# Kernel optimization log

Hardware: AMD Instinct MI355X
Metric: run time of the kernel (lower is better)

## Reference

```python
import jax, jax.numpy as jnp
import numpy as np

SPATIAL_SHAPES = [(128, 128), (64, 64), (32, 32), (16, 16)]
D_MODEL = 256
N_HEADS = 8
N_LEVELS = 4
N_POINTS = 4
HEAD_DIM = D_MODEL // N_HEADS
B = 2
LEN_Q = sum(h * w for h, w in SPATIAL_SHAPES)  # 21760
LEN_IN = LEN_Q


def setup_inputs() -> dict:
    key = jax.random.key(0)
    ks = jax.random.split(key, 11)
    s = 1.0 / np.sqrt(D_MODEL).astype(np.float32)
    query = jax.random.normal(ks[0], (B, LEN_Q, D_MODEL), jnp.float32)
    reference_points = jax.random.uniform(ks[1], (B, LEN_Q, N_LEVELS, 2), jnp.float32)
    input_flatten = jax.random.normal(ks[2], (B, LEN_IN, D_MODEL), jnp.float32)
    W_off = jax.random.normal(ks[3], (D_MODEL, N_HEADS * N_LEVELS * N_POINTS * 2), jnp.float32) * s
    b_off = jnp.zeros((N_HEADS * N_LEVELS * N_POINTS * 2,), jnp.float32)
    W_attn = jax.random.normal(ks[4], (D_MODEL, N_HEADS * N_LEVELS * N_POINTS), jnp.float32) * s
    b_attn = jnp.zeros((N_HEADS * N_LEVELS * N_POINTS,), jnp.float32)
    W_val = jax.random.normal(ks[5], (D_MODEL, D_MODEL), jnp.float32) * s
    b_val = jnp.zeros((D_MODEL,), jnp.float32)
    W_out = jax.random.normal(ks[6], (D_MODEL, D_MODEL), jnp.float32) * s
    b_out = jnp.zeros((D_MODEL,), jnp.float32)
    return {"query": query, "reference_points": reference_points, "input_flatten": input_flatten,
            "W_off": W_off, "b_off": b_off, "W_attn": W_attn, "b_attn": b_attn,
            "W_val": W_val, "b_val": b_val, "W_out": W_out, "b_out": b_out}


def _ms_deform_core(value, sampling_locations, attention_weights):
    # value: (B, H, Dh, N_total); sampling_locations: (B, Lq, H, L, P, 2) in [0,1]
    # attention_weights: (B, Lq, H, L*P)
    Bv, Hn, Dh, _ = value.shape
    Lq = sampling_locations.shape[1]
    P = sampling_locations.shape[4]
    BN = Bv * Hn
    grids = 2.0 * sampling_locations - 1.0
    splits = np.cumsum([h * w for h, w in SPATIAL_SHAPES])[:-1].tolist()
    value_list = jnp.split(value, splits, axis=3)
    sampled_levels = []
    for lid, (Hh, Ww) in enumerate(SPATIAL_SHAPES):
        # (BN, H*W, Dh)
        val_flat = jnp.transpose(value_list[lid].reshape(BN, Dh, Hh * Ww), (0, 2, 1))
        # (BN, Lq, P, 2)
        g = jnp.transpose(grids[:, :, :, lid, :, :], (0, 2, 1, 3, 4)).reshape(BN, Lq, P, 2)
        ix = ((g[..., 0] + 1.0) * Ww - 1.0) / 2.0
        iy = ((g[..., 1] + 1.0) * Hh - 1.0) / 2.0
        ix0 = jnp.floor(ix).astype(jnp.int32)
        iy0 = jnp.floor(iy).astype(jnp.int32)
        ix1 = ix0 + 1
        iy1 = iy0 + 1
        fx = (ix - ix0.astype(ix.dtype))[..., None]
        fy = (iy - iy0.astype(iy.dtype))[..., None]

        def valid(yy, xx):
            return ((xx >= 0) & (xx < Ww) & (yy >= 0) & (yy < Hh)).astype(val_flat.dtype)[..., None]

        def gather(yy, xx):
            idx = (jnp.clip(yy, 0, Hh - 1) * Ww + jnp.clip(xx, 0, Ww - 1)).reshape(BN, Lq * P)
            out = jnp.take_along_axis(val_flat, idx[:, :, None], axis=1)
            return out.reshape(BN, Lq, P, Dh)

        v00 = gather(iy0, ix0) * valid(iy0, ix0)
        v01 = gather(iy0, ix1) * valid(iy0, ix1)
        v10 = gather(iy1, ix0) * valid(iy1, ix0)
        v11 = gather(iy1, ix1) * valid(iy1, ix1)
        sampled = ((1 - fx) * (1 - fy) * v00 + fx * (1 - fy) * v01
                   + (1 - fx) * fy * v10 + fx * fy * v11)  # (BN, Lq, P, Dh)
        sampled_levels.append(jnp.transpose(sampled, (0, 3, 1, 2)))  # (BN, Dh, Lq, P)
    # (BN, Dh, Lq, L*P)
    sv = jnp.stack(sampled_levels, axis=-2).reshape(BN, Dh, Lq, N_LEVELS * P)
    attn = jnp.transpose(attention_weights, (0, 2, 1, 3)).reshape(BN, 1, Lq, N_LEVELS * P)
    out = jnp.sum(sv * attn, axis=-1)  # (BN, Dh, Lq)
    out = out.reshape(Bv, Hn * Dh, Lq)
    return jnp.transpose(out, (0, 2, 1))  # (B, Lq, d_model)


def reference(query, reference_points, input_flatten, W_off, b_off, W_attn, b_attn, W_val, b_val, W_out, b_out):
    Bq, Lq, _ = query.shape
    Len_in = input_flatten.shape[1]
    value = input_flatten @ W_val + b_val  # (B, Len_in, d_model)
    offsets = (query @ W_off + b_off).reshape(Bq, Lq, N_HEADS, N_LEVELS, N_POINTS, 2)
    attn = jax.nn.softmax((query @ W_attn + b_attn).reshape(Bq, Lq, N_HEADS, N_LEVELS * N_POINTS), axis=-1)
    # normalizer is (W, H) per level
    offset_normalizer = jnp.asarray([[w, h] for h, w in SPATIAL_SHAPES], dtype=query.dtype)
    sampling_locations = (reference_points[:, :, None, :, None, :]
                          + offsets / offset_normalizer[None, None, None, :, None, :])
    value = jnp.transpose(value, (0, 2, 1)).reshape(Bq, N_HEADS, HEAD_DIM, Len_in)
    out = _ms_deform_core(value, sampling_locations, attn)
    return out @ W_out + b_out
```

## Files before the change

kernel.cpp:

```cpp
#include <hip/hip_runtime.h>
#include <hip/hip_bf16.h>
#include <hip/hip_fp16.h>
#include <type_traits>

#define B_    2
#define LQ_   21760
#define LEN_  21760
#define DM    256
#define NH    8
#define NL    4
#define NP    4
#define HD    32

#define WS_VAL   0u
#define WS_SAMP  22282240u
#define WS_OA    44564480u
#define WS_WT    77987840u

typedef __attribute__((ext_vector_type(4))) float f32x4;
typedef __attribute__((ext_vector_type(8))) short bf16x8;
typedef __attribute__((ext_vector_type(4))) unsigned int u32x4;
typedef __attribute__((ext_vector_type(2))) unsigned int u32x2;

__device__ __forceinline__ unsigned short f2bf(float v) {
    __hip_bfloat16 h = __float2bfloat16(v);
    return *reinterpret_cast<unsigned short*>(&h);
}
__device__ __forceinline__ unsigned int pk2bf(float a, float b) {
    return (unsigned int)f2bf(a) | ((unsigned int)f2bf(b) << 16);
}
__device__ __forceinline__ unsigned int pk2h(float a, float b) {
    __half2 h = __floats2half2_rn(a, b);
    union { __half2 h; unsigned int u; } c; c.h = h; return c.u;
}
__device__ __forceinline__ __half2 u2h2(unsigned int u) {
    union { unsigned int u; __half2 h; } c; c.u = u; return c.h;
}

__global__ __launch_bounds__(256) void wt_cvt_all(const float* __restrict__ Wv,
                                                  const float* __restrict__ Wo,
                                                  const float* __restrict__ Wa,
                                                  const float* __restrict__ Wu,
                                                  unsigned short* __restrict__ wt) {
    const float* Ws[4] = {Wv, Wo, Wa, Wu};
    const int Ns[4] = {256, 256, 128, 256};
    const unsigned int dof[4] = {0u, 65536u, 131072u, 163840u};
    const int m = blockIdx.z;
    const int n0 = blockIdx.x * 16, k0 = blockIdx.y * 16;
    if (n0 >= Ns[m]) return;
    __shared__ float tile[16][17];
    const int tx = threadIdx.x & 15, ty = threadIdx.x >> 4;
    tile[ty][tx] = Ws[m][(size_t)(k0 + ty) * Ns[m] + n0 + tx];
    __syncthreads();
    wt[dof[m] + (size_t)(n0 + ty) * 256 + k0 + tx] = f2bf(tile[tx][ty]);
}

__global__ __launch_bounds__(256) void gemm_pre(const float* __restrict__ inpf,
                                                const float* __restrict__ query,
                                                const unsigned short* __restrict__ Wt_val,
                                                const unsigned short* __restrict__ Wt_oa,
                                                const float* __restrict__ b_val,
                                                const float* __restrict__ b_off,
                                                const float* __restrict__ b_attn,
                                                unsigned short* __restrict__ val_h,
                                                unsigned short* __restrict__ oa_h) {
    __shared__ unsigned short As[128 * 32];
    __shared__ unsigned short Bs[128 * 32];
    const int t = threadIdx.x;
    const int wv = t >> 6;
    const int ln = t & 63;
    const int job = (blockIdx.x >= 2);
    const int n0 = (job ? (blockIdx.x - 2) : blockIdx.x) * 128;
    const int m0 = blockIdx.y * 128;
    const float* A = job ? query : inpf;
    const unsigned short* Bt = job ? Wt_oa : Wt_val;
    const int K = 256;
    const int wm = (wv & 1) * 64;
    const int wn = (wv >> 1) * 64;
    const int lrow = ln & 15;
    const int kq = ln >> 4;

    f32x4 acc[4][4] = {};

    for (int k0 = 0; k0 < K; k0 += 32) {
#pragma unroll
        for (int c = 0; c < 4; ++c) {
            const int i = t + c * 256;
            const int row = i >> 3;
            const int kq4 = (i & 7) * 4;
            f32x4 v = *(const f32x4*)&A[(size_t)(m0 + row) * K + k0 + kq4];
            uint2 p = make_uint2(pk2bf(v.x, v.y), pk2bf(v.z, v.w));
            *(uint2*)((char*)As + row * 64 + kq4 * 2) = p;
        }
#pragma unroll
        for (int c = 0; c < 2; ++c) {
            const int o = c * 4096 + t * 16;
            const int row = o >> 6;
            const int ke = (o & 63) >> 1;
            const unsigned short* gb = Bt + (size_t)(n0 + row) * K + k0 + ke;
            __builtin_amdgcn_global_load_lds(
                (const __attribute__((address_space(1))) void*)gb,
                (__attribute__((address_space(3))) void*)((char*)Bs + o), 16, 0, 0);
        }
        __syncthreads();

        bf16x8 af[4], bfr[4];
#pragma unroll
        for (int i = 0; i < 4; ++i) {
            af[i]  = *(const bf16x8*)((char*)As + (wm + i * 16 + lrow) * 64 + kq * 16);
            bfr[i] = *(const bf16x8*)((char*)Bs + (wn + i * 16 + lrow) * 64 + kq * 16);
        }
#pragma unroll
        for (int i = 0; i < 4; ++i)
#pragma unroll
            for (int j = 0; j < 4; ++j)
                acc[i][j] = __builtin_amdgcn_mfma_f32_16x16x32_bf16(af[i], bfr[j], acc[i][j], 0, 0, 0);
        __syncthreads();
    }

    const int b = m0 / LQ_;
#pragma unroll
    for (int j = 0; j < 4; ++j) {
        const int n = n0 + wn + j * 16 + lrow;
        const float bb = job ? ((n < 256) ? b_off[n] : b_attn[n - 256]) : b_val[n];
#pragma unroll
        for (int i = 0; i < 4; ++i) {
            const int mrow = m0 + wm + i * 16 + kq * 4;
#pragma unroll
            for (int r = 0; r < 4; ++r) {
                const float v = acc[i][j][r] + bb;
                const unsigned short hv = (unsigned short)__half_as_ushort(__float2half(v));
                if (job) {
                    oa_h[(size_t)(mrow + r) * 384 + n] = hv;
                } else {
                    const int pix = (mrow + r) - b * LQ_;
                    const int h = n >> 5, c = n & 31;
                    val_h[((size_t)(b * NH + h) * LQ_ + pix) * HD + c] = hv;
                }
            }
        }
    }
}

__global__ __launch_bounds__(256) void gemm_out(const unsigned short* __restrict__ Ab,
                                                const unsigned short* __restrict__ Bt,
                                                const float* __restrict__ bias,
                                                float* __restrict__ C) {
    __shared__ unsigned short As[128 * 32];
    __shared__ unsigned short Bs[128 * 32];
    const int t = threadIdx.x;
    const int wv = t >> 6;
    const int ln = t & 63;
    const int n0 = blockIdx.x * 128;
    const int m0 = blockIdx.y * 128;
    const int N = 256, K = 256;
    const int wm = (wv & 1) * 64;
    const int wn = (wv >> 1) * 64;
    const int lrow = ln & 15;
    const int kq = ln >> 4;

    f32x4 acc[4][4] = {};

    for (int k0 = 0; k0 < K; k0 += 32) {
#pragma unroll
        for (int c = 0; c < 2; ++c) {
            const int o = c * 4096 + t * 16;
            const int row = o >> 6;
            const int ke = (o & 63) >> 1;
            const unsigned short* ga = Ab + (size_t)(m0 + row) * K + k0 + ke;
            const unsigned short* gb = Bt + (size_t)(n0 + row) * K + k0 + ke;
            __builtin_amdgcn_global_load_lds(
                (const __attribute__((address_space(1))) void*)ga,
                (__attribute__((address_space(3))) void*)((char*)As + o), 16, 0, 0);
            __builtin_amdgcn_global_load_lds(
                (const __attribute__((address_space(1))) void*)gb,
                (__attribute__((address_space(3))) void*)((char*)Bs + o), 16, 0, 0);
        }
        __syncthreads();

        bf16x8 af[4], bfr[4];
#pragma unroll
        for (int i = 0; i < 4; ++i) {
            af[i]  = *(const bf16x8*)((char*)As + (wm + i * 16 + lrow) * 64 + kq * 16);
            bfr[i] = *(const bf16x8*)((char*)Bs + (wn + i * 16 + lrow) * 64 + kq * 16);
        }
#pragma unroll
        for (int i = 0; i < 4; ++i)
#pragma unroll
            for (int j = 0; j < 4; ++j)
                acc[i][j] = __builtin_amdgcn_mfma_f32_16x16x32_bf16(af[i], bfr[j], acc[i][j], 0, 0, 0);
        __syncthreads();
    }

#pragma unroll
    for (int j = 0; j < 4; ++j) {
        const int n = n0 + wn + j * 16 + lrow;
        const float bb = bias[n];
#pragma unroll
        for (int i = 0; i < 4; ++i) {
            const int mrow = m0 + wm + i * 16 + kq * 4;
#pragma unroll
            for (int r = 0; r < 4; ++r)
                C[(size_t)(mrow + r) * N + n] = acc[i][j][r] + bb;
        }
    }
}

#define QB 4
__device__ __forceinline__ void accum4(const uint4& v, float w, float* acc) {
#pragma unroll
    for (int c = 0; c < 4; ++c) {
        const __half2 h = u2h2((&v.x)[c]);
        acc[c * 2]     = fmaf(w, __low2float(h),  acc[c * 2]);
        acc[c * 2 + 1] = fmaf(w, __high2float(h), acc[c * 2 + 1]);
    }
}

__global__ __launch_bounds__(256) void msda_sample5(const unsigned short* __restrict__ value,
                                                    const unsigned short* __restrict__ oa,
                                                    const float* __restrict__ refp,
                                                    unsigned short* __restrict__ samp) {
    __shared__ char smem[8320];
    unsigned int* s_pkw = (unsigned int*)smem;
    float* s_off   = (float*)smem;
    float* s_logit = (float*)(smem + 4096);
    float* s_aw    = (float*)(smem + 6144);
    float* s_ref   = (float*)(smem + 8192);

    const int t = threadIdx.x;
    const int j = blockIdx.x;
    const int bq0 = ((j & 7) * 1360 + (j >> 3)) * QB;
    const int b = bq0 / LQ_;

    {
        const unsigned short* oab = oa + (size_t)bq0 * 384;
        const int q = t >> 6, c = t & 63;
        u32x2 r0 = __builtin_nontemporal_load((const u32x2*)(oab + (size_t)q * 384) + c);
        float2 f0 = __half22float2(u2h2(r0.x));
        float2 f1 = __half22float2(u2h2(r0.y));
        f32x4 o0 = {f0.x, f0.y, f1.x, f1.y};
        ((f32x4*)s_off)[q * 64 + c] = o0;
        unsigned int r1 = __builtin_nontemporal_load((const unsigned int*)(oab + (size_t)q * 384 + 256) + c);
        float2 g0 = __half22float2(u2h2(r1));
        ((float2*)s_logit)[q * 64 + c] = make_float2(g0.x, g0.y);
        if (t < 8)
            ((f32x4*)s_ref)[t] = __builtin_nontemporal_load((const f32x4*)(refp + (size_t)bq0 * 8) + t);
    }
    __syncthreads();

    if (t < 32) {
        const float* lg = s_logit + (t >> 3) * 128 + (t & 7) * 16;
        float m = -1e30f;
#pragma unroll
        for (int i = 0; i < 16; ++i) m = fmaxf(m, lg[i]);
        float e[16], s = 0.f;
#pragma unroll
        for (int i = 0; i < 16; ++i) { e[i] = __expf(lg[i] - m); s += e[i]; }
        const float inv = 1.f / s;
#pragma unroll
        for (int i = 0; i < 16; ++i) s_aw[t * 16 + i] = e[i] * inv;
    }
    __syncthreads();

    uint4 ent[2];
    int wrd[2];
    {
        const int Wls[4] = {128, 64, 32, 16};
        const int Hls[4] = {128, 64, 32, 16};
        const int st_[4] = {0, 16384, 20480, 21504};
#pragma unroll
        for (int ii = 0; ii < 2; ++ii) {
            const int s = t * 2 + ii;
            const int q = s >> 7;
            const int rest = s & 127;
            const int h = rest >> 4;
            const int lp = rest & 15;
            const int l = lp >> 2;
            const int Wl = Wls[l], Hl = Hls[l], base = st_[l];
            const float ix = s_ref[q * 8 + l * 2]     * (float)Wl - 0.5f + s_off[q * 256 + rest * 2];
            const float iy = s_ref[q * 8 + l * 2 + 1] * (float)Hl - 0.5f + s_off[q * 256 + rest * 2 + 1];
            const float fix = floorf(ix), fiy = floorf(iy);
            const int x0 = (int)fix, y0 = (int)fiy;
            const float fx = ix - fix, fy = iy - fiy;
            int sx; float wl, wr;
            if (x0 < 0)            { sx = 0;      wl = (x0 == -1) ? fx : 0.f;        wr = 0.f; }
            else if (x0 >= Wl - 1) { sx = Wl - 2; wl = 0.f; wr = (x0 == Wl - 1) ? (1.f - fx) : 0.f; }
            else                   { sx = x0;     wl = 1.f - fx;                     wr = fx; }
            const float g0 = ((y0 >= 0) & (y0 < Hl)) ? (1.f - fy) : 0.f;
            const float g1 = ((y0 + 1 >= 0) & (y0 + 1 < Hl)) ? fy : 0.f;
            const int cy0 = min(max(y0, 0), Hl - 1);
            const int cy1 = min(max(y0 + 1, 0), Hl - 1);
            const float aw = s_aw[(q * 8 + h) * 16 + lp];
            ent[ii].x = (unsigned int)(base + cy0 * Wl + sx);
            ent[ii].y = (unsigned int)(base + cy1 * Wl + sx);
            ent[ii].z = pk2h(aw * wl * g0, aw * wr * g0);
            ent[ii].w = pk2h(aw * wl * g1, aw * wr * g1);
            wrd[ii] = q * 512 + lp * 32 + (((h ^ (lp & 7))) << 2);
        }
    }
    __syncthreads();

#pragma unroll
    for (int ii = 0; ii < 2; ++ii)
        *(uint4*)&s_pkw[wrd[ii]] = ent[ii];
    __syncthreads();

    const int q = t >> 6;
    const int lane = t & 63;
    const int h = lane >> 3;
    const int dg = lane & 7;
    const unsigned short* vb = value + ((size_t)(b * NH + h) * LQ_) * HD + dg * 8;

    float acc[8] = {0.f, 0.f, 0.f, 0.f, 0.f, 0.f, 0.f, 0.f};
#pragma unroll
    for (int lp = 0; lp < 16; ++lp) {
        const uint4 pk = *(const uint4*)&s_pkw[q * 512 + lp * 32 + ((h ^ (lp & 7)) << 2)];
        const uint4 v0 = *(const uint4*)(vb + (size_t)pk.x * HD);
        const uint4 v1 = *(const uint4*)(vb + (size_t)pk.y * HD);
        const __half2 w0 = u2h2(pk.z), w1 = u2h2(pk.w);
        const float f0 = (dg < 4) ? __low2float(w0) : __high2float(w0);
        const float f1 = (dg < 4) ? __low2float(w1) : __high2float(w1);
        accum4(v0, f0, acc);
        accum4(v1, f1, acc);
    }
#pragma unroll
    for (int i = 0; i < 8; ++i) acc[i] += __shfl_xor(acc[i], 4);

    if (dg < 4) {
        u32x4 o;
        o.x = pk2bf(acc[0], acc[1]);
        o.y = pk2bf(acc[2], acc[3]);
        o.z = pk2bf(acc[4], acc[5]);
        o.w = pk2bf(acc[6], acc[7]);
        __builtin_nontemporal_store(o, (u32x4*)(samp + (size_t)(bq0 + q) * 256 + h * HD + dg * 8));
    }
}

extern "C" void kernel_launch(void* const* d_in, const int* in_sizes, int n_in,
                              void* d_out, int out_size, void* d_ws, size_t ws_size,
                              hipStream_t stream) {
    const float* query  = (const float*)d_in[0];
    const float* refp   = (const float*)d_in[1];
    const float* inpf   = (const float*)d_in[2];
    const float* W_off  = (const float*)d_in[3];
    const float* b_off  = (const float*)d_in[4];
    const float* W_attn = (const float*)d_in[5];
    const float* b_attn = (const float*)d_in[6];
    const float* W_val  = (const float*)d_in[7];
    const float* b_val  = (const float*)d_in[8];
    const float* W_out  = (const float*)d_in[9];
    const float* b_out  = (const float*)d_in[10];
    float* out = (float*)d_out;

    char* ws = (char*)d_ws;
    unsigned short* val_h   = (unsigned short*)(ws + WS_VAL);
    unsigned short* samp_bf = (unsigned short*)(ws + WS_SAMP);
    unsigned short* oa_h    = (unsigned short*)(ws + WS_OA);
    unsigned short* wt      = (unsigned short*)(ws + WS_WT);
    unsigned short* Wt_val  = wt;
    unsigned short* Wt_oa   = wt + 65536;
    unsigned short* Wt_out  = wt + 163840;

    const int M = B_ * LQ_;

    wt_cvt_all<<<dim3(16, 16, 4), 256, 0, stream>>>(W_val, W_off, W_attn, W_out, wt);

    gemm_pre<<<dim3(5, M / 128), 256, 0, stream>>>(
        inpf, query, Wt_val, Wt_oa, b_val, b_off, b_attn, val_h, oa_h);

    msda_sample5<<<dim3(M / QB), 256, 0, stream>>>(val_h, oa_h, refp, samp_bf);

    gemm_out<<<dim3(2, M / 128), 256, 0, stream>>>(samp_bf, Wt_out, b_out, out);
}
```

Baseline: 289.6 us.

## Reorganize sampling kernel per head with half-precision FMA and load prefetch

```diff
diff --git a/kernel.cpp b/kernel.cpp
--- a/kernel.cpp
+++ b/kernel.cpp
@@ -206,21 +206,12 @@
     }
 }
 
-#define QB 4
-__device__ __forceinline__ void accum4(const uint4& v, float w, float* acc) {
-#pragma unroll
-    for (int c = 0; c < 4; ++c) {
-        const __half2 h = u2h2((&v.x)[c]);
-        acc[c * 2]     = fmaf(w, __low2float(h),  acc[c * 2]);
-        acc[c * 2 + 1] = fmaf(w, __high2float(h), acc[c * 2 + 1]);
-    }
-}
-
-__global__ __launch_bounds__(256) void msda_sample5(const unsigned short* __restrict__ value,
+#define QB6 32
+__global__ __launch_bounds__(256) void msda_sample6(const unsigned short* __restrict__ value,
                                                     const unsigned short* __restrict__ oa,
                                                     const float* __restrict__ refp,
                                                     unsigned short* __restrict__ samp) {
-    __shared__ char smem[8320];
+    __shared__ __align__(16) char smem[9216];
     unsigned int* s_pkw = (unsigned int*)smem;
     float* s_off   = (float*)smem;
     float* s_logit = (float*)(smem + 4096);
@@ -229,27 +220,29 @@
 
     const int t = threadIdx.x;
     const int j = blockIdx.x;
-    const int bq0 = ((j & 7) * 1360 + (j >> 3)) * QB;
-    const int b = bq0 / LQ_;
+    const int h = j & 7;
+    const int bqc = j >> 3;
+    const int b = (bqc >= 680);
+    const int q0 = (bqc - b * 680) * QB6;
+    const int bq0 = b * LQ_ + q0;
 
     {
-        const unsigned short* oab = oa + (size_t)bq0 * 384;
-        const int q = t >> 6, c = t & 63;
-        u32x2 r0 = __builtin_nontemporal_load((const u32x2*)(oab + (size_t)q * 384) + c);
+        const int q = t >> 3, c = t & 7;
+        const unsigned short* oab = oa + (size_t)(bq0 + q) * 384;
+        u32x2 r0 = __builtin_nontemporal_load((const u32x2*)(oab + h * 32) + c);
         float2 f0 = __half22float2(u2h2(r0.x));
         float2 f1 = __half22float2(u2h2(r0.y));
         f32x4 o0 = {f0.x, f0.y, f1.x, f1.y};
-        ((f32x4*)s_off)[q * 64 + c] = o0;
-        unsigned int r1 = __builtin_nontemporal_load((const unsigned int*)(oab + (size_t)q * 384 + 256) + c);
+        ((f32x4*)s_off)[q * 8 + c] = o0;
+        unsigned int r1 = __builtin_nontemporal_load((const unsigned int*)(oab + 256 + h * 16) + c);
         float2 g0 = __half22float2(u2h2(r1));
-        ((float2*)s_logit)[q * 64 + c] = make_float2(g0.x, g0.y);
-        if (t < 8)
-            ((f32x4*)s_ref)[t] = __builtin_nontemporal_load((const f32x4*)(refp + (size_t)bq0 * 8) + t);
+        ((float2*)s_logit)[q * 8 + c] = make_float2(g0.x, g0.y);
+        s_ref[q * 8 + c] = __builtin_nontemporal_load(refp + (size_t)(bq0 + q) * 8 + c);
     }
     __syncthreads();
 
     if (t < 32) {
-        const float* lg = s_logit + (t >> 3) * 128 + (t & 7) * 16;
+        const float* lg = s_logit + t * 16;
         float m = -1e30f;
 #pragma unroll
         for (int i = 0; i < 16; ++i) m = fmaxf(m, lg[i]);
@@ -271,14 +264,12 @@
 #pragma unroll
         for (int ii = 0; ii < 2; ++ii) {
             const int s = t * 2 + ii;
-            const int q = s >> 7;
-            const int rest = s & 127;
-            const int h = rest >> 4;
-            const int lp = rest & 15;
+            const int q = s >> 4;
+            const int lp = s & 15;
             const int l = lp >> 2;
             const int Wl = Wls[l], Hl = Hls[l], base = st_[l];
-            const float ix = s_ref[q * 8 + l * 2]     * (float)Wl - 0.5f + s_off[q * 256 + rest * 2];
-            const float iy = s_ref[q * 8 + l * 2 + 1] * (float)Hl - 0.5f + s_off[q * 256 + rest * 2 + 1];
+            const float ix = s_ref[q * 8 + l * 2]     * (float)Wl - 0.5f + s_off[q * 32 + lp * 2];
+            const float iy = s_ref[q * 8 + l * 2 + 1] * (float)Hl - 0.5f + s_off[q * 32 + lp * 2 + 1];
             const float fix = floorf(ix), fiy = floorf(iy);
             const int x0 = (int)fix, y0 = (int)fiy;
             const float fx = ix - fix, fy = iy - fiy;
@@ -290,12 +281,12 @@
             const float g1 = ((y0 + 1 >= 0) & (y0 + 1 < Hl)) ? fy : 0.f;
             const int cy0 = min(max(y0, 0), Hl - 1);
             const int cy1 = min(max(y0 + 1, 0), Hl - 1);
-            const float aw = s_aw[(q * 8 + h) * 16 + lp];
+            const float aw = s_aw[q * 16 + lp];
             ent[ii].x = (unsigned int)(base + cy0 * Wl + sx);
             ent[ii].y = (unsigned int)(base + cy1 * Wl + sx);
             ent[ii].z = pk2h(aw * wl * g0, aw * wr * g0);
             ent[ii].w = pk2h(aw * wl * g1, aw * wr * g1);
-            wrd[ii] = q * 512 + lp * 32 + (((h ^ (lp & 7))) << 2);
+            wrd[ii] = q * 64 + ((lp ^ (q & 7)) << 2);
         }
     }
     __syncthreads();
@@ -305,33 +296,60 @@
         *(uint4*)&s_pkw[wrd[ii]] = ent[ii];
     __syncthreads();
 
-    const int q = t >> 6;
     const int lane = t & 63;
-    const int h = lane >> 3;
+    const int wv = t >> 6;
+    const int ql = lane >> 3;
+    const int q = wv * 8 + ql;
     const int dg = lane & 7;
     const unsigned short* vb = value + ((size_t)(b * NH + h) * LQ_) * HD + dg * 8;
-
-    float acc[8] = {0.f, 0.f, 0.f, 0.f, 0.f, 0.f, 0.f, 0.f};
+    const unsigned int wsel = (dg < 4) ? 0x01000100u : 0x03020302u;
+    const int wb = q * 64 + (ql << 2);
+
+    float facc[8] = {0.f, 0.f, 0.f, 0.f, 0.f, 0.f, 0.f, 0.f};
+    __half2 ah[4] = {u2h2(0u), u2h2(0u), u2h2(0u), u2h2(0u)};
+
+    uint4 pk = *(const uint4*)&s_pkw[wb];
+    uint4 va0 = *(const uint4*)(vb + (size_t)pk.x * HD);
+    uint4 va1 = *(const uint4*)(vb + (size_t)pk.y * HD);
+    unsigned int wz = pk.z, ww = pk.w;
+
 #pragma unroll
     for (int lp = 0; lp < 16; ++lp) {
-        const uint4 pk = *(const uint4*)&s_pkw[q * 512 + lp * 32 + ((h ^ (lp & 7)) << 2)];
-        const uint4 v0 = *(const uint4*)(vb + (size_t)pk.x * HD);
-        const uint4 v1 = *(const uint4*)(vb + (size_t)pk.y * HD);
-        const __half2 w0 = u2h2(pk.z), w1 = u2h2(pk.w);
-        const float f0 = (dg < 4) ? __low2float(w0) : __high2float(w0);
-        const float f1 = (dg < 4) ? __low2float(w1) : __high2float(w1);
-        accum4(v0, f0, acc);
-        accum4(v1, f1, acc);
-    }
-#pragma unroll
-    for (int i = 0; i < 8; ++i) acc[i] += __shfl_xor(acc[i], 4);
+        const uint4 cv0 = va0, cv1 = va1;
+        const unsigned int cz = wz, cw = ww;
+        if (lp < 15) {
+            uint4 pn = *(const uint4*)&s_pkw[wb ^ ((lp + 1) << 2)];
+            wz = pn.z; ww = pn.w;
+            va0 = *(const uint4*)(vb + (size_t)pn.x * HD);
+            va1 = *(const uint4*)(vb + (size_t)pn.y * HD);
+        }
+        const __half2 w0 = u2h2(__builtin_amdgcn_perm(cz, cz, wsel));
+        const __half2 w1 = u2h2(__builtin_amdgcn_perm(cw, cw, wsel));
+#pragma unroll
+        for (int c2 = 0; c2 < 4; ++c2) {
+            ah[c2] = __hfma2(w0, u2h2((&cv0.x)[c2]), ah[c2]);
+            ah[c2] = __hfma2(w1, u2h2((&cv1.x)[c2]), ah[c2]);
+        }
+        if ((lp & 3) == 3) {
+#pragma unroll
+            for (int c2 = 0; c2 < 4; ++c2) {
+                float2 f = __half22float2(ah[c2]);
+                facc[c2 * 2]     += f.x;
+                facc[c2 * 2 + 1] += f.y;
+                ah[c2] = u2h2(0u);
+            }
+        }
+    }
+
+#pragma unroll
+    for (int i = 0; i < 8; ++i) facc[i] += __shfl_xor(facc[i], 4);
 
     if (dg < 4) {
         u32x4 o;
-        o.x = pk2bf(acc[0], acc[1]);
-        o.y = pk2bf(acc[2], acc[3]);
-        o.z = pk2bf(acc[4], acc[5]);
-        o.w = pk2bf(acc[6], acc[7]);
+        o.x = pk2bf(facc[0], facc[1]);
+        o.y = pk2bf(facc[2], facc[3]);
+        o.z = pk2bf(facc[4], facc[5]);
+        o.w = pk2bf(facc[6], facc[7]);
         __builtin_nontemporal_store(o, (u32x4*)(samp + (size_t)(bq0 + q) * 256 + h * HD + dg * 8));
     }
 }
@@ -368,7 +386,7 @@
     gemm_pre<<<dim3(5, M / 128), 256, 0, stream>>>(
         inpf, query, Wt_val, Wt_oa, b_val, b_off, b_attn, val_h, oa_h);
 
-    msda_sample5<<<dim3(M / QB), 256, 0, stream>>>(val_h, oa_h, refp, samp_bf);
+    msda_sample6<<<dim3(B_ * NH * (LQ_ / QB6)), 256, 0, stream>>>(val_h, oa_h, refp, samp_bf);
 
     gemm_out<<<dim3(2, M / 128), 256, 0, stream>>>(samp_bf, Wt_out, b_out, out);
 }
```

After: 286.6 us. Within noise of the previous version (-1.0%).
